# Kernel tuning notes

Measured on AMD Instinct MI355X. Metric: run time of the kernel, lower is better.

Reference implementation:

```python
import jax, jax.numpy as jnp
import numpy as np

N_NODES = 100000
N_EDGES = 1600000
DIM = 64
N_GRAPHS = 1000


def setup_inputs() -> dict:
    key = jax.random.key(0)
    ks = jax.random.split(key, 6)
    s = 1.0 / np.sqrt(DIM)
    x = jax.random.normal(ks[0], (N_NODES, DIM), dtype=jnp.float32)
    edge_index = jax.random.randint(ks[1], (2, N_EDGES), 0, N_NODES, dtype=jnp.int64)
    batch = jnp.sort(jax.random.randint(ks[2], (N_NODES,), 0, N_GRAPHS, dtype=jnp.int64))
    W1 = jax.random.normal(ks[3], (DIM, DIM), dtype=jnp.float32) * s
    b1 = jnp.zeros((DIM,), jnp.float32)
    W2 = jax.random.normal(ks[4], (DIM, DIM), dtype=jnp.float32) * s
    b2 = jnp.zeros((DIM,), jnp.float32)
    return {"x": x, "W1": W1, "b1": b1, "W2": W2, "b2": b2,
            "edge_index": edge_index, "batch": batch}


def reference(x, W1, b1, W2, b2, edge_index, batch):
    n = x.shape[0]
    loop = jnp.arange(n, dtype=edge_index.dtype)
    src = jnp.concatenate([edge_index[0], loop])  # [E+N] with self-loops
    dst = jnp.concatenate([edge_index[1], loop])
    # symmetric GCN normalization: deg^{-1/2}[src] * deg^{-1/2}[dst]
    deg = jax.ops.segment_sum(jnp.ones(src.shape[0], x.dtype), dst, num_segments=n)
    dinv = jax.lax.rsqrt(jnp.maximum(deg, 1.0))  # deg >= 1 due to self-loops
    norm = (dinv[src] * dinv[dst])[:, None]      # [E+N, 1]

    def gcn(h, W, b):
        h = h @ W                                  # transform first (smaller dim path)
        msg = h[src] * norm                        # gather + normalize
        return jax.ops.segment_sum(msg, dst, num_segments=n) + b

    h = jax.nn.relu(gcn(x, W1, b1))
    # dropout: eval mode -> identity
    h = jax.nn.relu(gcn(h, W2, b2))

    counts = jax.ops.segment_sum(jnp.ones((n,), x.dtype), batch, num_segments=N_GRAPHS)
    pooled = jax.ops.segment_sum(h, batch, num_segments=N_GRAPHS)
    return pooled / jnp.maximum(counts, 1.0)[:, None]
```

## Files before the change

kernel.cpp:

```cpp
#include <hip/hip_runtime.h>
#include <hip/hip_fp16.h>

#define DIM 64
#define BIN_SHIFT 7
#define BINSZ 128
#define MAXBINS 1024
#define PB 512
#define PB_LOG 9

typedef __attribute__((ext_vector_type(2))) float floatx2;
typedef __attribute__((ext_vector_type(4))) float f32x4;
typedef __attribute__((ext_vector_type(8))) _Float16 f16x8;
typedef __attribute__((ext_vector_type(4))) _Float16 f16x4;


__global__ __launch_bounds__(256) void k_hist(const int* __restrict__ dst,
                                              int* __restrict__ C, int E, int NB) {
    __shared__ int h[MAXBINS];
    for (int i = threadIdx.x; i < NB; i += 256) h[i] = 0;
    __syncthreads();
    int per = (E + PB - 1) / PB;
    int e0 = blockIdx.x * per;
    int e1 = e0 + per; if (e1 > E) e1 = E;
    for (int e = e0 + (int)threadIdx.x; e < e1; e += 256)
        atomicAdd(&h[dst[e] >> BIN_SHIFT], 1);
    __syncthreads();
    for (int i = threadIdx.x; i < NB; i += 256)
        C[blockIdx.x * NB + i] = h[i];
}


__global__ __launch_bounds__(1024) void k_scanA(const int* __restrict__ C,
                                                int* __restrict__ S,
                                                int* __restrict__ bsums, int NB, int M) {
    __shared__ int sh[1024];
    int tid = threadIdx.x;
    int j0 = blockIdx.x * 4096 + tid * 4;
    int v[4]; int sum = 0;
#pragma unroll
    for (int t = 0; t < 4; ++t) {
        int j = j0 + t; int x = 0;
        if (j < M) { int bin = j >> PB_LOG, blk = j & (PB - 1); x = C[blk * NB + bin]; }
        v[t] = sum; sum += x;
    }
    sh[tid] = sum;
    __syncthreads();
#pragma unroll
    for (int d = 1; d < 1024; d <<= 1) {
        int t = (tid >= d) ? sh[tid - d] : 0;
        __syncthreads();
        sh[tid] += t;
        __syncthreads();
    }
    int excl = sh[tid] - sum;
#pragma unroll
    for (int t = 0; t < 4; ++t) {
        int j = j0 + t;
        if (j < M) S[j] = excl + v[t];
    }
    if (tid == 1023) bsums[blockIdx.x] = sh[1023];
}


__global__ __launch_bounds__(1024) void k_scanB(int* __restrict__ bsums, int nb) {
    __shared__ int s[1024];
    int tid = threadIdx.x;
    int v = (tid < nb) ? bsums[tid] : 0;
    s[tid] = v;
    __syncthreads();
#pragma unroll
    for (int d = 1; d < 1024; d <<= 1) {
        int t = (tid >= d) ? s[tid - d] : 0;
        __syncthreads();
        s[tid] += t;
        __syncthreads();
    }
    if (tid < nb) bsums[tid] = s[tid] - v;
}


__global__ __launch_bounds__(256) void k_bucket(const int* __restrict__ src,
                                                const int* __restrict__ dst,
                                                const int* __restrict__ S,
                                                const int* __restrict__ bsums,
                                                int* __restrict__ bkt, int E, int NB) {
    __shared__ int lcur[MAXBINS];
    int blk = blockIdx.x;
    for (int i = threadIdx.x; i < NB; i += 256) {
        int j = i * PB + blk;
        lcur[i] = S[j] + bsums[j >> 12];
    }
    __syncthreads();
    int per = (E + PB - 1) / PB;
    int e0 = blk * per;
    int e1 = e0 + per; if (e1 > E) e1 = E;
    for (int e = e0 + (int)threadIdx.x; e < e1; e += 256) {
        int d = dst[e];
        int pos = atomicAdd(&lcur[d >> BIN_SHIFT], 1);
        bkt[pos] = src[e] | ((d & (BINSZ - 1)) << 24);
    }
}


__global__ __launch_bounds__(256) void k_binsort(const int* __restrict__ bkt,
                                                 const int* __restrict__ S,
                                                 const int* __restrict__ bsums,
                                                 int* __restrict__ csr,
                                                 int* __restrict__ off,
                                                 float* __restrict__ dinv,
                                                 const int* __restrict__ batch,
                                                 int* __restrict__ goff,
                                                 float* __restrict__ outz,
                                                 int N, int G, int E, int NB) {
    __shared__ int cnt[BINSZ], bas[BINSZ], cur[BINSZ];
    __shared__ int wsum[4];
    int tid = threadIdx.x;
    int b = blockIdx.x;
    for (int i = b * 256 + tid; i < G * DIM; i += NB * 256) outz[i] = 0.f;
    int j0 = b << PB_LOG;
    int s0 = S[j0] + bsums[j0 >> 12];
    int s1 = E;
    if (b + 1 < NB) { int j1 = (b + 1) << PB_LOG; s1 = S[j1] + bsums[j1 >> 12]; }
    if (tid < BINSZ) { cnt[tid] = 0; cur[tid] = 0; }
    __syncthreads();
    for (int i = s0 + tid; i < s1; i += 256)
        atomicAdd(&cnt[(bkt[i] >> 24) & (BINSZ - 1)], 1);
    __syncthreads();
    int my = (tid < BINSZ) ? cnt[tid] : 0;
    int lane = tid & 63, wv = tid >> 6;
    int x = my;
#pragma unroll
    for (int d = 1; d < 64; d <<= 1) {
        int t = __shfl_up(x, d);
        if (lane >= d) x += t;
    }
    if (lane == 63) wsum[wv] = x;
    __syncthreads();
    int prefix = 0;
    for (int w = 0; w < wv; ++w) prefix += wsum[w];
    int ex = x + prefix - my;
    if (tid < BINSZ) {
        bas[tid] = ex;
        int v = (b << BIN_SHIFT) + tid;
        if (v < N) {
            off[v] = s0 + ex;
            dinv[v] = rsqrtf((float)(my + 1));
            if (v == N - 1) off[N] = E;
            int bb = batch[v];
            int prev = (v == 0) ? -1 : batch[v - 1];
            for (int g = prev + 1; g <= bb; ++g) goff[g] = v;
            if (v == N - 1)
                for (int g = bb + 1; g <= G; ++g) goff[g] = N;
        }
    }
    __syncthreads();
    for (int i = s0 + tid; i < s1; i += 256) {
        int p = bkt[i];
        int lo = (p >> 24) & (BINSZ - 1);
        int li = atomicAdd(&cur[lo], 1);
        csr[s0 + bas[lo] + li] = p & 0xFFFFFF;
    }
}


__global__ __launch_bounds__(256) void k_gemm(const float* __restrict__ X,
                                              const float* __restrict__ W,
                                              const float* __restrict__ dinv,
                                              unsigned int* __restrict__ Y8, int N) {
    __shared__ float Os[16 * 68];
    int tid = threadIdx.x;
    int lane = tid & 63, w = tid >> 6;
    int m = lane & 15, g = lane >> 4;
    int row0 = blockIdx.x * 16;
    int row = row0 + m;

    f16x8 B0, B1;
    {
        int n = (w << 4) + m;
        const float* wp = W + (g << 3) * 64 + n;
#pragma unroll
        for (int j = 0; j < 8; ++j) B0[j] = (_Float16)wp[j * 64];
        wp += 32 * 64;
#pragma unroll
        for (int j = 0; j < 8; ++j) B1[j] = (_Float16)wp[j * 64];
    }
    f16x8 A0, A1;
    {
        float4 u0 = make_float4(0.f, 0.f, 0.f, 0.f), u1 = u0, u2 = u0, u3 = u0;
        if (row < N) {
            const float* xp = X + (size_t)row * DIM + (g << 3);
            u0 = *(const float4*)(xp);
            u1 = *(const float4*)(xp + 4);
            u2 = *(const float4*)(xp + 32);
            u3 = *(const float4*)(xp + 36);
        }
        A0[0] = (_Float16)u0.x; A0[1] = (_Float16)u0.y; A0[2] = (_Float16)u0.z; A0[3] = (_Float16)u0.w;
        A0[4] = (_Float16)u1.x; A0[5] = (_Float16)u1.y; A0[6] = (_Float16)u1.z; A0[7] = (_Float16)u1.w;
        A1[0] = (_Float16)u2.x; A1[1] = (_Float16)u2.y; A1[2] = (_Float16)u2.z; A1[3] = (_Float16)u2.w;
        A1[4] = (_Float16)u3.x; A1[5] = (_Float16)u3.y; A1[6] = (_Float16)u3.z; A1[7] = (_Float16)u3.w;
    }
    f32x4 acc = {0.f, 0.f, 0.f, 0.f};
    acc = __builtin_amdgcn_mfma_f32_16x16x32_f16(A0, B0, acc, 0, 0, 0);
    acc = __builtin_amdgcn_mfma_f32_16x16x32_f16(A1, B1, acc, 0, 0, 0);
#pragma unroll
    for (int j = 0; j < 4; ++j)
        Os[((g << 2) + j) * 68 + (w << 4) + m] = acc[j];
    __syncthreads();

    int r = tid >> 4, c = tid & 15;
    int orow = row0 + r;
    if (orow < N) {
        float4 o = *(const float4*)(Os + r * 68 + (c << 2));
        float s = dinv[orow];
        int p = 0;
        p = __builtin_amdgcn_cvt_pk_fp8_f32(o.x * s, o.y * s, p, false);
        p = __builtin_amdgcn_cvt_pk_fp8_f32(o.z * s, o.w * s, p, true);
        Y8[(size_t)orow * 16 + c] = (unsigned int)p;
    } else if (orow == N) {
        Y8[(size_t)orow * 16 + c] = 0u;
    }
}


__device__ __forceinline__ float4 gather_rows(const unsigned int* __restrict__ hs8,
                                              const int* __restrict__ csr,
                                              int k0, int k1, int v, int l, int gw4,
                                              int N) {
    float4 a0, a1, a2, a3;
    {
        unsigned int u = hs8[(unsigned)((v << 4) | l)];
        floatx2 f0 = __builtin_amdgcn_cvt_pk_f32_fp8((int)u, false);
        floatx2 f1 = __builtin_amdgcn_cvt_pk_f32_fp8((int)u, true);
        a0 = make_float4(f0.x, f0.y, f1.x, f1.y);
        a1 = make_float4(0.f, 0.f, 0.f, 0.f);
        a2 = make_float4(0.f, 0.f, 0.f, 0.f);
        a3 = make_float4(0.f, 0.f, 0.f, 0.f);
    }
    for (int kb = k0; kb < k1; kb += 16) {
        int rem = k1 - kb;
        int idx = (l < rem) ? csr[kb + l] : N;
        unsigned uu[16];
#pragma unroll
        for (int t = 0; t < 16; ++t) {
            int s = __shfl(idx, gw4 + t);
            uu[t] = hs8[(unsigned)((s << 4) | l)];
        }
#pragma unroll
        for (int t = 0; t < 16; t += 4) {
            floatx2 q0 = __builtin_amdgcn_cvt_pk_f32_fp8((int)uu[t + 0], false);
            floatx2 q1 = __builtin_amdgcn_cvt_pk_f32_fp8((int)uu[t + 0], true);
            floatx2 q2 = __builtin_amdgcn_cvt_pk_f32_fp8((int)uu[t + 1], false);
            floatx2 q3 = __builtin_amdgcn_cvt_pk_f32_fp8((int)uu[t + 1], true);
            floatx2 q4 = __builtin_amdgcn_cvt_pk_f32_fp8((int)uu[t + 2], false);
            floatx2 q5 = __builtin_amdgcn_cvt_pk_f32_fp8((int)uu[t + 2], true);
            floatx2 q6 = __builtin_amdgcn_cvt_pk_f32_fp8((int)uu[t + 3], false);
            floatx2 q7 = __builtin_amdgcn_cvt_pk_f32_fp8((int)uu[t + 3], true);
            a0.x += q0.x; a0.y += q0.y; a0.z += q1.x; a0.w += q1.y;
            a1.x += q2.x; a1.y += q2.y; a1.z += q3.x; a1.w += q3.y;
            a2.x += q4.x; a2.y += q4.y; a2.z += q5.x; a2.w += q5.y;
            a3.x += q6.x; a3.y += q6.y; a3.z += q7.x; a3.w += q7.y;
        }
    }
    return make_float4(a0.x + a1.x + a2.x + a3.x,
                       a0.y + a1.y + a2.y + a3.y,
                       a0.z + a1.z + a2.z + a3.z,
                       a0.w + a1.w + a2.w + a3.w);
}


__global__ __launch_bounds__(256) void k_gather_gemm(const unsigned int* __restrict__ hs8,
                                                     const int* __restrict__ csr,
                                                     const int* __restrict__ off,
                                                     const float* __restrict__ dinv,
                                                     const float* __restrict__ bias,
                                                     const float* __restrict__ W,
                                                     unsigned int* __restrict__ hs_out,
                                                     int N) {
    __shared__ _Float16 Xs[16 * 72];
    __shared__ float Os[16 * 68];
    int tid = threadIdx.x;
    int r = tid >> 4, l = tid & 15;
    int lane = tid & 63, w = tid >> 6;
    int m = lane & 15, g = lane >> 4;
    int gw4 = (r & 3) << 4;
    int v = blockIdx.x * 16 + r;

    f16x8 B0, B1;
    {
        int n = (w << 4) + m;
        const float* wp = W + (g << 3) * 64 + n;
#pragma unroll
        for (int j = 0; j < 8; ++j) B0[j] = (_Float16)wp[j * 64];
        wp += 32 * 64;
#pragma unroll
        for (int j = 0; j < 8; ++j) B1[j] = (_Float16)wp[j * 64];
    }
    if (blockIdx.x == 0 && tid < 16)
        hs_out[(size_t)N * 16 + tid] = 0u;

    float dv = 0.f;
    float4 h = make_float4(0.f, 0.f, 0.f, 0.f);
    if (v < N) {
        dv = dinv[v];
        float4 bv = ((const float4*)bias)[l];
        float4 acc = gather_rows(hs8, csr, off[v], off[v + 1], v, l, gw4, N);
        h.x = fmaxf(acc.x * dv + bv.x, 0.f);
        h.y = fmaxf(acc.y * dv + bv.y, 0.f);
        h.z = fmaxf(acc.z * dv + bv.z, 0.f);
        h.w = fmaxf(acc.w * dv + bv.w, 0.f);
    }
    {
        f16x4 hv;
        hv[0] = (_Float16)h.x; hv[1] = (_Float16)h.y;
        hv[2] = (_Float16)h.z; hv[3] = (_Float16)h.w;
        *(f16x4*)(Xs + r * 72 + (l << 2)) = hv;
    }
    __syncthreads();

    f16x8 A0 = *(const f16x8*)(Xs + m * 72 + (g << 3));
    f16x8 A1 = *(const f16x8*)(Xs + m * 72 + 32 + (g << 3));
    f32x4 acc2 = {0.f, 0.f, 0.f, 0.f};
    acc2 = __builtin_amdgcn_mfma_f32_16x16x32_f16(A0, B0, acc2, 0, 0, 0);
    acc2 = __builtin_amdgcn_mfma_f32_16x16x32_f16(A1, B1, acc2, 0, 0, 0);
#pragma unroll
    for (int j = 0; j < 4; ++j)
        Os[((g << 2) + j) * 68 + (w << 4) + m] = acc2[j];
    __syncthreads();

    if (v < N) {
        float4 o = *(const float4*)(Os + r * 68 + (l << 2));
        int p = 0;
        p = __builtin_amdgcn_cvt_pk_fp8_f32(o.x * dv, o.y * dv, p, false);
        p = __builtin_amdgcn_cvt_pk_fp8_f32(o.z * dv, o.w * dv, p, true);
        hs_out[(size_t)v * 16 + l] = (unsigned int)p;
    }
}


__global__ __launch_bounds__(256) void k_gather_pool(const unsigned int* __restrict__ hs8,
                                                     const int* __restrict__ csr,
                                                     const int* __restrict__ off,
                                                     const float* __restrict__ dinv,
                                                     const float* __restrict__ bias,
                                                     const int* __restrict__ batch,
                                                     const int* __restrict__ goff,
                                                     float* __restrict__ out, int N) {
    __shared__ float vals[16][68];
    __shared__ int gid[16];
    int tid = threadIdx.x;
    int r = tid >> 4, l = tid & 15;
    int gw4 = (r & 3) << 4;
    int v = blockIdx.x * 16 + r;

    float4 val = make_float4(0.f, 0.f, 0.f, 0.f);
    int g = -1;
    if (v < N) {
        g = batch[v];
        float dv = dinv[v];
        float4 bv = ((const float4*)bias)[l];
        float4 acc = gather_rows(hs8, csr, off[v], off[v + 1], v, l, gw4, N);
        float inv = 1.0f / (float)(goff[g + 1] - goff[g]);
        val.x = fmaxf(acc.x * dv + bv.x, 0.f) * inv;
        val.y = fmaxf(acc.y * dv + bv.y, 0.f) * inv;
        val.z = fmaxf(acc.z * dv + bv.z, 0.f) * inv;
        val.w = fmaxf(acc.w * dv + bv.w, 0.f) * inv;
    }
    *(float4*)(&vals[r][l << 2]) = val;
    if (l == 0) gid[r] = g;
    __syncthreads();

    if (v < N) {
        bool leader = (r == 0) || (gid[r - 1] != g);
        if (leader) {
            float4 s = val;
            for (int rr = r + 1; rr < 16 && gid[rr] == g; ++rr) {
                float4 t = *(const float4*)(&vals[rr][l << 2]);
                s.x += t.x; s.y += t.y; s.z += t.z; s.w += t.w;
            }
            float* op = out + (size_t)g * DIM + (l << 2);
            atomicAdd(op + 0, s.x);
            atomicAdd(op + 1, s.y);
            atomicAdd(op + 2, s.z);
            atomicAdd(op + 3, s.w);
        }
    }
}


static inline int cdiv(int a, int b) { return (a + b - 1) / b; }

extern "C" void kernel_launch(void* const* d_in, const int* in_sizes, int n_in,
                              void* d_out, int out_size, void* d_ws, size_t ws_size,
                              hipStream_t stream) {
    const float* x   = (const float*)d_in[0];
    const float* W1  = (const float*)d_in[1];
    const float* b1  = (const float*)d_in[2];
    const float* W2  = (const float*)d_in[3];
    const float* b2  = (const float*)d_in[4];
    const int*   ei  = (const int*)d_in[5];
    const int*   bat = (const int*)d_in[6];

    const int N = in_sizes[0] / DIM;
    const int E = in_sizes[5] / 2;
    const int G = out_size / DIM;
    const int NB = cdiv(N, BINSZ);
    const int M  = NB * PB;
    const int* src = ei;
    const int* dst = ei + E;
    float* out = (float*)d_out;

    __half* hs1    = (__half*)d_ws;
    __half* hs2    = hs1 + (size_t)(N + 1) * DIM;
    __half* spare  = hs2 + (size_t)(N + 1) * DIM;
    float*  dinv   = (float*)(spare + (size_t)N * DIM);
    int*    off    = (int*)(dinv + N);
    int*    goff   = off + (N + 1);
    int*    C      = goff + (G + 1);
    int*    S      = C + (size_t)PB * NB;
    int*    bsums  = S + (size_t)PB * NB;
    int*    csr    = bsums + 1024;
    int*    bkt    = (int*)hs1;

    k_hist<<<PB, 256, 0, stream>>>(dst, C, E, NB);
    int nb2 = cdiv(M, 4096);
    k_scanA<<<nb2, 1024, 0, stream>>>(C, S, bsums, NB, M);
    k_scanB<<<1, 1024, 0, stream>>>(bsums, nb2);
    k_bucket<<<PB, 256, 0, stream>>>(src, dst, S, bsums, bkt, E, NB);
    k_binsort<<<NB, 256, 0, stream>>>(bkt, S, bsums, csr, off, dinv, bat, goff,
                                      out, N, G, E, NB);

    k_gemm<<<cdiv(N + 1, 16), 256, 0, stream>>>(x, W1, dinv, (unsigned int*)hs1, N);

    k_gather_gemm<<<cdiv(N, 16), 256, 0, stream>>>((const unsigned int*)hs1, csr, off,
                                                   dinv, b1, W2, (unsigned int*)hs2, N);

    k_gather_pool<<<cdiv(N, 16), 256, 0, stream>>>((const unsigned int*)hs2, csr, off,
                                                   dinv, b2, bat, goff, out, N);
}
```

Measured before the change: 197.2 us.

## Gather fp8 rows with 8-byte loads split across half-groups and prefetch CSR

The edge gather now has each 16-lane group split into two halves. Each half loads 8-byte chunks of a different neighbor row, so every lane issues 8 wider loads per 16 edges instead of 16 narrow ones. The two halves' partial sums are combined with a cross-lane xor shuffle, and the next block of CSR indices is prefetched while the current loads are in flight. Output column mapping is permuted (c4g) in the consumers to match the new lane-to-column assignment. The change adds shuffle reductions and a permuted column layout in exchange for fewer load instructions per edge.

```diff
diff --git a/kernel.cpp b/kernel.cpp
--- a/kernel.cpp
+++ b/kernel.cpp
@@ -226,45 +226,46 @@
                                               const int* __restrict__ csr,
                                               int k0, int k1, int v, int l, int gw4,
                                               int N) {
-    float4 a0, a1, a2, a3;
-    {
-        unsigned int u = hs8[(unsigned)((v << 4) | l)];
-        floatx2 f0 = __builtin_amdgcn_cvt_pk_f32_fp8((int)u, false);
-        floatx2 f1 = __builtin_amdgcn_cvt_pk_f32_fp8((int)u, true);
-        a0 = make_float4(f0.x, f0.y, f1.x, f1.y);
-        a1 = make_float4(0.f, 0.f, 0.f, 0.f);
-        a2 = make_float4(0.f, 0.f, 0.f, 0.f);
-        a3 = make_float4(0.f, 0.f, 0.f, 0.f);
-    }
-    for (int kb = k0; kb < k1; kb += 16) {
-        int rem = k1 - kb;
-        int idx = (l < rem) ? csr[kb + l] : N;
-        unsigned uu[16];
-#pragma unroll
-        for (int t = 0; t < 16; ++t) {
-            int s = __shfl(idx, gw4 + t);
-            uu[t] = hs8[(unsigned)((s << 4) | l)];
+    int p = l >> 3, s = l & 7;
+    float4 alo = make_float4(0.f, 0.f, 0.f, 0.f);
+    float4 ahi = make_float4(0.f, 0.f, 0.f, 0.f);
+    if (p == 0) {
+        uint2 u = *(const uint2*)(hs8 + (((unsigned)v << 4) | (s << 1)));
+        floatx2 f0 = __builtin_amdgcn_cvt_pk_f32_fp8((int)u.x, false);
+        floatx2 f1 = __builtin_amdgcn_cvt_pk_f32_fp8((int)u.x, true);
+        floatx2 f2 = __builtin_amdgcn_cvt_pk_f32_fp8((int)u.y, false);
+        floatx2 f3 = __builtin_amdgcn_cvt_pk_f32_fp8((int)u.y, true);
+        alo = make_float4(f0.x, f0.y, f1.x, f1.y);
+        ahi = make_float4(f2.x, f2.y, f3.x, f3.y);
+    }
+    int kb = k0;
+    int idx = N;
+    if (kb < k1) idx = (l < k1 - kb) ? csr[kb + l] : N;
+    while (kb < k1) {
+        int nkb = kb + 16;
+        uint2 uu[8];
+#pragma unroll
+        for (int t = 0; t < 8; ++t) {
+            int e = __shfl(idx, gw4 + (t << 1) + p);
+            uu[t] = *(const uint2*)(hs8 + (((unsigned)e << 4) | (s << 1)));
         }
-#pragma unroll
-        for (int t = 0; t < 16; t += 4) {
-            floatx2 q0 = __builtin_amdgcn_cvt_pk_f32_fp8((int)uu[t + 0], false);
-            floatx2 q1 = __builtin_amdgcn_cvt_pk_f32_fp8((int)uu[t + 0], true);
-            floatx2 q2 = __builtin_amdgcn_cvt_pk_f32_fp8((int)uu[t + 1], false);
-            floatx2 q3 = __builtin_amdgcn_cvt_pk_f32_fp8((int)uu[t + 1], true);
-            floatx2 q4 = __builtin_amdgcn_cvt_pk_f32_fp8((int)uu[t + 2], false);
-            floatx2 q5 = __builtin_amdgcn_cvt_pk_f32_fp8((int)uu[t + 2], true);
-            floatx2 q6 = __builtin_amdgcn_cvt_pk_f32_fp8((int)uu[t + 3], false);
-            floatx2 q7 = __builtin_amdgcn_cvt_pk_f32_fp8((int)uu[t + 3], true);
-            a0.x += q0.x; a0.y += q0.y; a0.z += q1.x; a0.w += q1.y;
-            a1.x += q2.x; a1.y += q2.y; a1.z += q3.x; a1.w += q3.y;
-            a2.x += q4.x; a2.y += q4.y; a2.z += q5.x; a2.w += q5.y;
-            a3.x += q6.x; a3.y += q6.y; a3.z += q7.x; a3.w += q7.y;
+        if (nkb < k1) idx = (l < k1 - nkb) ? csr[nkb + l] : N;
+#pragma unroll
+        for (int t = 0; t < 8; ++t) {
+            floatx2 f0 = __builtin_amdgcn_cvt_pk_f32_fp8((int)uu[t].x, false);
+            floatx2 f1 = __builtin_amdgcn_cvt_pk_f32_fp8((int)uu[t].x, true);
+            floatx2 f2 = __builtin_amdgcn_cvt_pk_f32_fp8((int)uu[t].y, false);
+            floatx2 f3 = __builtin_amdgcn_cvt_pk_f32_fp8((int)uu[t].y, true);
+            alo.x += f0.x; alo.y += f0.y; alo.z += f1.x; alo.w += f1.y;
+            ahi.x += f2.x; ahi.y += f2.y; ahi.z += f3.x; ahi.w += f3.y;
         }
-    }
-    return make_float4(a0.x + a1.x + a2.x + a3.x,
-                       a0.y + a1.y + a2.y + a3.y,
-                       a0.z + a1.z + a2.z + a3.z,
-                       a0.w + a1.w + a2.w + a3.w);
+        kb = nkb;
+    }
+    alo.x += __shfl_xor(alo.x, 8); alo.y += __shfl_xor(alo.y, 8);
+    alo.z += __shfl_xor(alo.z, 8); alo.w += __shfl_xor(alo.w, 8);
+    ahi.x += __shfl_xor(ahi.x, 8); ahi.y += __shfl_xor(ahi.y, 8);
+    ahi.z += __shfl_xor(ahi.z, 8); ahi.w += __shfl_xor(ahi.w, 8);
+    return p ? ahi : alo;
 }
 
 
@@ -280,6 +281,7 @@
     __shared__ float Os[16 * 68];
     int tid = threadIdx.x;
     int r = tid >> 4, l = tid & 15;
+    int c4g = ((l & 7) << 1) | (l >> 3);
     int lane = tid & 63, w = tid >> 6;
     int m = lane & 15, g = lane >> 4;
     int gw4 = (r & 3) << 4;
@@ -302,7 +304,7 @@
     float4 h = make_float4(0.f, 0.f, 0.f, 0.f);
     if (v < N) {
         dv = dinv[v];
-        float4 bv = ((const float4*)bias)[l];
+        float4 bv = ((const float4*)bias)[c4g];
         float4 acc = gather_rows(hs8, csr, off[v], off[v + 1], v, l, gw4, N);
         h.x = fmaxf(acc.x * dv + bv.x, 0.f);
         h.y = fmaxf(acc.y * dv + bv.y, 0.f);
@@ -313,7 +315,7 @@
         f16x4 hv;
         hv[0] = (_Float16)h.x; hv[1] = (_Float16)h.y;
         hv[2] = (_Float16)h.z; hv[3] = (_Float16)h.w;
-        *(f16x4*)(Xs + r * 72 + (l << 2)) = hv;
+        *(f16x4*)(Xs + r * 72 + (c4g << 2)) = hv;
     }
     __syncthreads();
 
@@ -328,11 +330,11 @@
     __syncthreads();
 
     if (v < N) {
-        float4 o = *(const float4*)(Os + r * 68 + (l << 2));
+        float4 o = *(const float4*)(Os + r * 68 + (c4g << 2));
         int p = 0;
         p = __builtin_amdgcn_cvt_pk_fp8_f32(o.x * dv, o.y * dv, p, false);
         p = __builtin_amdgcn_cvt_pk_fp8_f32(o.z * dv, o.w * dv, p, true);
-        hs_out[(size_t)v * 16 + l] = (unsigned int)p;
+        hs_out[(size_t)v * 16 + c4g] = (unsigned int)p;
     }
 }
 
@@ -349,6 +351,7 @@
     __shared__ int gid[16];
     int tid = threadIdx.x;
     int r = tid >> 4, l = tid & 15;
+    int c4g = ((l & 7) << 1) | (l >> 3);
     int gw4 = (r & 3) << 4;
     int v = blockIdx.x * 16 + r;
 
@@ -357,7 +360,7 @@
     if (v < N) {
         g = batch[v];
         float dv = dinv[v];
-        float4 bv = ((const float4*)bias)[l];
+        float4 bv = ((const float4*)bias)[c4g];
         float4 acc = gather_rows(hs8, csr, off[v], off[v + 1], v, l, gw4, N);
         float inv = 1.0f / (float)(goff[g + 1] - goff[g]);
         val.x = fmaxf(acc.x * dv + bv.x, 0.f) * inv;
@@ -365,23 +368,23 @@
         val.z = fmaxf(acc.z * dv + bv.z, 0.f) * inv;
         val.w = fmaxf(acc.w * dv + bv.w, 0.f) * inv;
     }
-    *(float4*)(&vals[r][l << 2]) = val;
+    *(float4*)(&vals[r][c4g << 2]) = val;
     if (l == 0) gid[r] = g;
     __syncthreads();
 
     if (v < N) {
         bool leader = (r == 0) || (gid[r - 1] != g);
         if (leader) {
-            float4 s = val;
+            float4 sacc = val;
             for (int rr = r + 1; rr < 16 && gid[rr] == g; ++rr) {
-                float4 t = *(const float4*)(&vals[rr][l << 2]);
-                s.x += t.x; s.y += t.y; s.z += t.z; s.w += t.w;
+                float4 t = *(const float4*)(&vals[rr][c4g << 2]);
+                sacc.x += t.x; sacc.y += t.y; sacc.z += t.z; sacc.w += t.w;
             }
-            float* op = out + (size_t)g * DIM + (l << 2);
-            atomicAdd(op + 0, s.x);
-            atomicAdd(op + 1, s.y);
-            atomicAdd(op + 2, s.z);
-            atomicAdd(op + 3, s.w);
+            float* op = out + (size_t)g * DIM + (c4g << 2);
+            atomicAdd(op + 0, sacc.x);
+            atomicAdd(op + 1, sacc.y);
+            atomicAdd(op + 2, sacc.z);
+            atomicAdd(op + 3, sacc.w);
         }
     }
 }
```

After: 197.8 us. No clear change (+0.3%).

## Replace per-block histogram scan with global bin totals and atomic bucket reservation

Applied to the files above, without the earlier changes.

The two-level scan over a per-block × per-bin count matrix (512×782 entries) is replaced. Each block now atomically adds its local histogram into a global bin-total array, a single small block scans the 782 totals, and the bucketing kernel recounts its chunk locally and reserves per-bin ranges with one global atomic per bin. This removes the large count-matrix write and read and one scan launch, at the cost of recounting dst in the bucket kernel, adding a zeroing kernel, and making the edge order within a bin nondeterministic.

```diff
diff --git a/kernel.cpp b/kernel.cpp
--- a/kernel.cpp
+++ b/kernel.cpp
@@ -6,7 +6,6 @@
 #define BINSZ 128
 #define MAXBINS 1024
 #define PB 512
-#define PB_LOG 9
 
 typedef __attribute__((ext_vector_type(2))) float floatx2;
 typedef __attribute__((ext_vector_type(4))) float f32x4;
@@ -14,8 +13,17 @@
 typedef __attribute__((ext_vector_type(4))) _Float16 f16x4;
 
 
-__global__ __launch_bounds__(256) void k_hist(const int* __restrict__ dst,
-                                              int* __restrict__ C, int E, int NB) {
+__global__ __launch_bounds__(256) void k_zero(int* __restrict__ bintot,
+                                              float* __restrict__ out,
+                                              int NB, int GD) {
+    int i = blockIdx.x * 256 + threadIdx.x;
+    if (i < NB) bintot[i] = 0;
+    for (int j = i; j < GD; j += gridDim.x * 256) out[j] = 0.f;
+}
+
+
+__global__ __launch_bounds__(256) void k_hist2(const int* __restrict__ dst,
+                                               int* __restrict__ bintot, int E, int NB) {
     __shared__ int h[MAXBINS];
     for (int i = threadIdx.x; i < NB; i += 256) h[i] = 0;
     __syncthreads();
@@ -26,101 +34,87 @@
         atomicAdd(&h[dst[e] >> BIN_SHIFT], 1);
     __syncthreads();
     for (int i = threadIdx.x; i < NB; i += 256)
-        C[blockIdx.x * NB + i] = h[i];
-}
-
-
-__global__ __launch_bounds__(1024) void k_scanA(const int* __restrict__ C,
-                                                int* __restrict__ S,
-                                                int* __restrict__ bsums, int NB, int M) {
-    __shared__ int sh[1024];
-    int tid = threadIdx.x;
-    int j0 = blockIdx.x * 4096 + tid * 4;
+        if (h[i]) atomicAdd(&bintot[i], h[i]);
+}
+
+
+__global__ __launch_bounds__(256) void k_scan782(const int* __restrict__ bintot,
+                                                 int* __restrict__ binoff,
+                                                 int* __restrict__ bincur, int NB, int E) {
+    __shared__ int ws[4];
+    int tid = threadIdx.x;
+    int j0 = tid * 4;
     int v[4]; int sum = 0;
-#pragma unroll
-    for (int t = 0; t < 4; ++t) {
-        int j = j0 + t; int x = 0;
-        if (j < M) { int bin = j >> PB_LOG, blk = j & (PB - 1); x = C[blk * NB + bin]; }
-        v[t] = sum; sum += x;
-    }
-    sh[tid] = sum;
-    __syncthreads();
-#pragma unroll
-    for (int d = 1; d < 1024; d <<= 1) {
-        int t = (tid >= d) ? sh[tid - d] : 0;
-        __syncthreads();
-        sh[tid] += t;
-        __syncthreads();
-    }
-    int excl = sh[tid] - sum;
 #pragma unroll
     for (int t = 0; t < 4; ++t) {
         int j = j0 + t;
-        if (j < M) S[j] = excl + v[t];
-    }
-    if (tid == 1023) bsums[blockIdx.x] = sh[1023];
-}
-
-
-__global__ __launch_bounds__(1024) void k_scanB(int* __restrict__ bsums, int nb) {
-    __shared__ int s[1024];
-    int tid = threadIdx.x;
-    int v = (tid < nb) ? bsums[tid] : 0;
-    s[tid] = v;
-    __syncthreads();
-#pragma unroll
-    for (int d = 1; d < 1024; d <<= 1) {
-        int t = (tid >= d) ? s[tid - d] : 0;
-        __syncthreads();
-        s[tid] += t;
-        __syncthreads();
-    }
-    if (tid < nb) bsums[tid] = s[tid] - v;
-}
-
-
-__global__ __launch_bounds__(256) void k_bucket(const int* __restrict__ src,
-                                                const int* __restrict__ dst,
-                                                const int* __restrict__ S,
-                                                const int* __restrict__ bsums,
-                                                int* __restrict__ bkt, int E, int NB) {
-    __shared__ int lcur[MAXBINS];
-    int blk = blockIdx.x;
-    for (int i = threadIdx.x; i < NB; i += 256) {
-        int j = i * PB + blk;
-        lcur[i] = S[j] + bsums[j >> 12];
-    }
+        int x = (j < NB) ? bintot[j] : 0;
+        v[t] = sum; sum += x;
+    }
+    int lane = tid & 63, wv = tid >> 6;
+    int x = sum;
+#pragma unroll
+    for (int d = 1; d < 64; d <<= 1) {
+        int t = __shfl_up(x, d);
+        if (lane >= d) x += t;
+    }
+    if (lane == 63) ws[wv] = x;
+    __syncthreads();
+    int prefix = 0;
+    for (int w = 0; w < wv; ++w) prefix += ws[w];
+    int ex = prefix + x - sum;
+#pragma unroll
+    for (int t = 0; t < 4; ++t) {
+        int j = j0 + t;
+        if (j < NB) { binoff[j] = ex + v[t]; bincur[j] = ex + v[t]; }
+    }
+    if (tid == 255) binoff[NB] = prefix + x;
+}
+
+
+__global__ __launch_bounds__(256) void k_bucket2(const int* __restrict__ src,
+                                                 const int* __restrict__ dst,
+                                                 int* __restrict__ bincur,
+                                                 int* __restrict__ bkt, int E, int NB) {
+    __shared__ int cnt_[MAXBINS], base_[MAXBINS];
+    int tid = threadIdx.x;
+    for (int i = tid; i < NB; i += 256) cnt_[i] = 0;
     __syncthreads();
     int per = (E + PB - 1) / PB;
-    int e0 = blk * per;
+    int e0 = blockIdx.x * per;
     int e1 = e0 + per; if (e1 > E) e1 = E;
-    for (int e = e0 + (int)threadIdx.x; e < e1; e += 256) {
+    for (int e = e0 + tid; e < e1; e += 256)
+        atomicAdd(&cnt_[dst[e] >> BIN_SHIFT], 1);
+    __syncthreads();
+    for (int i = tid; i < NB; i += 256) {
+        int c = cnt_[i];
+        base_[i] = c ? atomicAdd(&bincur[i], c) : 0;
+        cnt_[i] = 0;
+    }
+    __syncthreads();
+    for (int e = e0 + tid; e < e1; e += 256) {
         int d = dst[e];
-        int pos = atomicAdd(&lcur[d >> BIN_SHIFT], 1);
+        int b = d >> BIN_SHIFT;
+        int pos = base_[b] + atomicAdd(&cnt_[b], 1);
         bkt[pos] = src[e] | ((d & (BINSZ - 1)) << 24);
     }
 }
 
 
 __global__ __launch_bounds__(256) void k_binsort(const int* __restrict__ bkt,
-                                                 const int* __restrict__ S,
-                                                 const int* __restrict__ bsums,
+                                                 const int* __restrict__ binoff,
                                                  int* __restrict__ csr,
                                                  int* __restrict__ off,
                                                  float* __restrict__ dinv,
                                                  const int* __restrict__ batch,
                                                  int* __restrict__ goff,
-                                                 float* __restrict__ outz,
                                                  int N, int G, int E, int NB) {
     __shared__ int cnt[BINSZ], bas[BINSZ], cur[BINSZ];
     __shared__ int wsum[4];
     int tid = threadIdx.x;
     int b = blockIdx.x;
-    for (int i = b * 256 + tid; i < G * DIM; i += NB * 256) outz[i] = 0.f;
-    int j0 = b << PB_LOG;
-    int s0 = S[j0] + bsums[j0 >> 12];
-    int s1 = E;
-    if (b + 1 < NB) { int j1 = (b + 1) << PB_LOG; s1 = S[j1] + bsums[j1 >> 12]; }
+    int s0 = binoff[b];
+    int s1 = binoff[b + 1];
     if (tid < BINSZ) { cnt[tid] = 0; cur[tid] = 0; }
     __syncthreads();
     for (int i = s0 + tid; i < s1; i += 256)
@@ -372,16 +366,16 @@
     if (v < N) {
         bool leader = (r == 0) || (gid[r - 1] != g);
         if (leader) {
-            float4 s = val;
+            float4 sacc = val;
             for (int rr = r + 1; rr < 16 && gid[rr] == g; ++rr) {
                 float4 t = *(const float4*)(&vals[rr][l << 2]);
-                s.x += t.x; s.y += t.y; s.z += t.z; s.w += t.w;
+                sacc.x += t.x; sacc.y += t.y; sacc.z += t.z; sacc.w += t.w;
             }
             float* op = out + (size_t)g * DIM + (l << 2);
-            atomicAdd(op + 0, s.x);
-            atomicAdd(op + 1, s.y);
-            atomicAdd(op + 2, s.z);
-            atomicAdd(op + 3, s.w);
+            atomicAdd(op + 0, sacc.x);
+            atomicAdd(op + 1, sacc.y);
+            atomicAdd(op + 2, sacc.z);
+            atomicAdd(op + 3, sacc.w);
         }
     }
 }
@@ -404,30 +398,26 @@
     const int E = in_sizes[5] / 2;
     const int G = out_size / DIM;
     const int NB = cdiv(N, BINSZ);
-    const int M  = NB * PB;
     const int* src = ei;
     const int* dst = ei + E;
     float* out = (float*)d_out;
 
     __half* hs1    = (__half*)d_ws;
     __half* hs2    = hs1 + (size_t)(N + 1) * DIM;
-    __half* spare  = hs2 + (size_t)(N + 1) * DIM;
-    float*  dinv   = (float*)(spare + (size_t)N * DIM);
+    float*  dinv   = (float*)(hs2 + (size_t)(N + 1) * DIM);
     int*    off    = (int*)(dinv + N);
     int*    goff   = off + (N + 1);
-    int*    C      = goff + (G + 1);
-    int*    S      = C + (size_t)PB * NB;
-    int*    bsums  = S + (size_t)PB * NB;
-    int*    csr    = bsums + 1024;
+    int*    bintot = goff + (G + 1);
+    int*    binoff = bintot + MAXBINS;
+    int*    bincur = binoff + (MAXBINS + 1);
+    int*    csr    = bincur + MAXBINS;
     int*    bkt    = (int*)hs1;
 
-    k_hist<<<PB, 256, 0, stream>>>(dst, C, E, NB);
-    int nb2 = cdiv(M, 4096);
-    k_scanA<<<nb2, 1024, 0, stream>>>(C, S, bsums, NB, M);
-    k_scanB<<<1, 1024, 0, stream>>>(bsums, nb2);
-    k_bucket<<<PB, 256, 0, stream>>>(src, dst, S, bsums, bkt, E, NB);
-    k_binsort<<<NB, 256, 0, stream>>>(bkt, S, bsums, csr, off, dinv, bat, goff,
-                                      out, N, G, E, NB);
+    k_zero<<<256, 256, 0, stream>>>(bintot, out, NB, G * DIM);
+    k_hist2<<<PB, 256, 0, stream>>>(dst, bintot, E, NB);
+    k_scan782<<<1, 256, 0, stream>>>(bintot, binoff, bincur, NB, E);
+    k_bucket2<<<PB, 256, 0, stream>>>(src, dst, bincur, bkt, E, NB);
+    k_binsort<<<NB, 256, 0, stream>>>(bkt, binoff, csr, off, dinv, bat, goff, N, G, E, NB);
 
     k_gemm<<<cdiv(N + 1, 16), 256, 0, stream>>>(x, W1, dinv, (unsigned int*)hs1, N);
 
```

Measured after the change: 218.9 us. +11.0%, slower.
